# Kernel optimization log

Hardware: AMD Instinct MI355X
Metric: run time of the kernel (lower is better)

Reference implementation:

```python
import jax, jax.numpy as jnp
import numpy as np

ENC = 512            # encoder_image_size
RADIUS = 5.0         # user_input_circle_radius
B, Q, P = 4, 8, 4
IN_H, IN_W = 1024, 1024


def setup_inputs() -> dict:
    key = jax.random.key(0)
    k1, k2, k3 = jax.random.split(key, 3)
    batched_images = jax.random.uniform(k1, (B, 3, IN_H, IN_W), dtype=jnp.float32)
    # points in pixel coordinates of the input image
    batched_points = jax.random.uniform(k2, (B, Q, P, 2), dtype=jnp.float32) * jnp.float32(IN_W)
    batched_point_labels = jax.random.randint(k3, (B, Q, P), 0, 4, dtype=jnp.int32)
    pixel_mean = jnp.array([0.485, 0.456, 0.406], dtype=jnp.float32).reshape(1, 3, 1, 1)
    pixel_std = jnp.array([0.229, 0.224, 0.225], dtype=jnp.float32).reshape(1, 3, 1, 1)
    return {
        "batched_images": batched_images,
        "batched_points": batched_points,
        "batched_point_labels": batched_point_labels,
        "pixel_mean": pixel_mean,
        "pixel_std": pixel_std,
    }


def _early_fusion(batched_images, batched_points, batched_point_labels, pixel_mean, pixel_std):
    b, _, in_h, in_w = batched_images.shape
    q = batched_points.shape[1]
    S = ENC
    # preprocess: bilinear resize (align_corners=False) + normalize
    x = jax.image.resize(batched_images, (b, 3, S, S), method="bilinear", antialias=False)
    x = (x - pixel_mean) / pixel_std
    # rescale points to encoder resolution, keeping negatives at -1
    px = jnp.where(batched_points[..., 0] >= 0, batched_points[..., 0] * (S / in_w), -1.0)
    py = jnp.where(batched_points[..., 1] >= 0, batched_points[..., 1] * (S / in_h), -1.0)
    pts = jnp.stack([px, py], axis=-1)                      # [B,Q,P,2]

    rows = jnp.arange(S, dtype=jnp.float32)                 # row ids (y)
    cols = jnp.arange(S, dtype=jnp.float32)                 # col ids (x)

    # bbox mask from first two points if label[...,0] != 1, else full image
    is_bbox = (batched_point_labels[:, :, 0] != 1).astype(jnp.float32)   # [B,Q]
    tlx = is_bbox * jnp.min(pts[:, :, :2, 0], axis=-1)
    tly = is_bbox * jnp.min(pts[:, :, :2, 1], axis=-1)
    brx = is_bbox * jnp.max(pts[:, :, :2, 0], axis=-1) + (1.0 - is_bbox) * S
    bry = is_bbox * jnp.max(pts[:, :, :2, 1], axis=-1) + (1.0 - is_bbox) * S
    row_within = (rows[None, None, :, None] >= tly[:, :, None, None]) & (rows[None, None, :, None] <= bry[:, :, None, None])
    col_within = (cols[None, None, None, :] >= tlx[:, :, None, None]) & (cols[None, None, None, :] <= brx[:, :, None, None])
    bbox_mask = (row_within & col_within).astype(x.dtype)   # [B,Q,S,S]

    # point (circle) mask: min over points of squared distance, gated by label==1
    is_point = (batched_point_labels == 1).astype(jnp.float32)[:, :, None, None, :]   # [B,Q,1,1,P]
    dx = cols[None, None, None, :, None] - pts[:, :, None, None, :, 0]  # [B,Q,1,S,P]
    dy = rows[None, None, :, None, None] - pts[:, :, None, None, :, 1]  # [B,Q,S,1,P]
    d2 = dx * dx + dy * dy                                               # [B,Q,S,S,P]
    r2 = RADIUS * RADIUS
    gated = d2 * is_point + (1.0 - is_point) * (r2 + 1.0)
    pts_mask = (jnp.min(gated, axis=-1) <= r2).astype(x.dtype)          # [B,Q,S,S]

    imgs = jnp.broadcast_to(x[:, None], (b, q, 3, S, S))
    fused = jnp.concatenate([imgs, bbox_mask[:, :, None], pts_mask[:, :, None]], axis=2)
    return fused.reshape(b * q, 5, S, S)


def reference(batched_images, batched_points, batched_point_labels, pixel_mean, pixel_std):
    return _early_fusion(batched_images, batched_points, batched_point_labels, pixel_mean, pixel_std)
```

## Files before the change

kernel.cpp:

```cpp
#include <hip/hip_runtime.h>

#define S_ENC 512
#define IN_WH 1024
#define NB 4
#define NQ 8
#define NPTS 4
#define PLANE_STRIDE (5 * S_ENC * S_ENC)

typedef float f32x4 __attribute__((ext_vector_type(4)));

__global__ __launch_bounds__(256) void early_fusion_kernel(
    const float* __restrict__ img,
    const float* __restrict__ pts,
    const int*   __restrict__ labels,
    const float* __restrict__ mean,
    const float* __restrict__ stdv,
    float* __restrict__ out)
{
  const int job = blockIdx.y;
  const int tid = blockIdx.x * 256 + threadIdx.x;
  const int y   = tid >> 7;
  const int x4  = (tid & 127) << 2;

  if (job < NB * 3) {
    const int bc = job;
    const int b  = bc / 3;
    const int c  = bc % 3;
    const float m = mean[c];
    const float s = stdv[c];

    const float* in0 =
        img + ((size_t)bc * IN_WH + (size_t)(2 * y)) * IN_WH + 2 * x4;
    const f32x4 a0 = __builtin_nontemporal_load((const f32x4*)(in0));
    const f32x4 a1 = __builtin_nontemporal_load((const f32x4*)(in0 + 4));
    const f32x4 b0 = __builtin_nontemporal_load((const f32x4*)(in0 + IN_WH));
    const f32x4 b1 = __builtin_nontemporal_load((const f32x4*)(in0 + IN_WH + 4));

    f32x4 r;
    r.x = 0.5f * (0.5f * (a0.x + a0.y) + 0.5f * (b0.x + b0.y));
    r.y = 0.5f * (0.5f * (a0.z + a0.w) + 0.5f * (b0.z + b0.w));
    r.z = 0.5f * (0.5f * (a1.x + a1.y) + 0.5f * (b1.x + b1.y));
    r.w = 0.5f * (0.5f * (a1.z + a1.w) + 0.5f * (b1.z + b1.w));
    r.x = (r.x - m) / s;
    r.y = (r.y - m) / s;
    r.z = (r.z - m) / s;
    r.w = (r.w - m) / s;

    float* dst = out + ((size_t)(b * NQ * 5 + c) * S_ENC + y) * S_ENC + x4;
#pragma unroll
    for (int q = 0; q < NQ; ++q) {
      __builtin_nontemporal_store(r, (f32x4*)dst);
      dst += PLANE_STRIDE;
    }
  } else {
    const int idx = job - NB * 3;
    const int bq  = idx >> 1;
    const int c   = 3 + (idx & 1);

    const float* p   = pts + (size_t)bq * NPTS * 2;
    const int*   lab = labels + (size_t)bq * NPTS;
    float px[NPTS], py[NPTS];
    int   lb[NPTS];
#pragma unroll
    for (int i = 0; i < NPTS; ++i) {
      const float vx = p[2 * i + 0];
      const float vy = p[2 * i + 1];
      px[i] = (vx >= 0.0f) ? __fmul_rn(vx, 0.5f) : -1.0f;
      py[i] = (vy >= 0.0f) ? __fmul_rn(vy, 0.5f) : -1.0f;
      lb[i] = lab[i];
    }
    const float fy = (float)y;
    f32x4 r;

    if (c == 3) {
      float tlx, tly, brx, bry;
      if (lb[0] != 1) {
        tlx = fminf(px[0], px[1]);
        tly = fminf(py[0], py[1]);
        brx = fmaxf(px[0], px[1]);
        bry = fmaxf(py[0], py[1]);
      } else {
        tlx = 0.0f; tly = 0.0f;
        brx = (float)S_ENC; bry = (float)S_ENC;
      }
      const bool rowok = (fy >= tly) && (fy <= bry);
#pragma unroll
      for (int j = 0; j < 4; ++j) {
        const float fx = (float)(x4 + j);
        r[j] = (rowok && fx >= tlx && fx <= brx) ? 1.0f : 0.0f;
      }
    } else {
#pragma unroll
      for (int j = 0; j < 4; ++j) {
        const float fx = (float)(x4 + j);
        float mind = 26.0f;
#pragma unroll
        for (int i = 0; i < NPTS; ++i) {
          if (lb[i] == 1) {
            const float dx = __fsub_rn(fx, px[i]);
            const float dy = __fsub_rn(fy, py[i]);
            const float d2 = __fadd_rn(__fmul_rn(dx, dx), __fmul_rn(dy, dy));
            mind = fminf(mind, d2);
          }
        }
        r[j] = (mind <= 25.0f) ? 1.0f : 0.0f;
      }
    }

    __builtin_nontemporal_store(
        r, (f32x4*)(out + ((size_t)(bq * 5 + c) * S_ENC + y) * S_ENC + x4));
  }
}

extern "C" void kernel_launch(void* const* d_in, const int* in_sizes, int n_in,
                              void* d_out, int out_size, void* d_ws, size_t ws_size,
                              hipStream_t stream) {
  const float* img    = (const float*)d_in[0];
  const float* pts    = (const float*)d_in[1];
  const int*   labels = (const int*)d_in[2];
  const float* mean   = (const float*)d_in[3];
  const float* stdv   = (const float*)d_in[4];
  float* out = (float*)d_out;

  dim3 grid(256, NB * 3 + NB * NQ * 2);
  early_fusion_kernel<<<grid, 256, 0, stream>>>(img, pts, labels, mean, stdv, out);
}
```

Baseline: 40.48 us.

## Flatten grid, drop nontemporal hints, widen mask work per thread

Replaces the 2D grid with a 1D grid where image blocks come first and mask jobs use 64 blocks each, with every mask thread writing four float4 chunks 128 columns apart. Nontemporal loads and stores are swapped for ordinary vector loads and stores. The aim is to cut the number of mask blocks and their per-block setup (point and label loads), and to let normal caching handle the write-heavy output. The cost is less parallelism in the mask phase and possible cache pollution from the regular stores.

After: 36.08 us. 1.12x faster.

```diff
diff --git a/kernel.cpp b/kernel.cpp
--- a/kernel.cpp
+++ b/kernel.cpp
@@ -9,6 +9,12 @@
 
 typedef float f32x4 __attribute__((ext_vector_type(4)));
 
+#define IMG_JOBS   (NB * 3)
+#define IMG_BLOCKS (IMG_JOBS * 256)
+#define MASK_JOBS  (NB * NQ * 2)
+#define MASK_BLK_PER_JOB 64
+#define MASK_BLOCKS (MASK_JOBS * MASK_BLK_PER_JOB)
+
 __global__ __launch_bounds__(256) void early_fusion_kernel(
     const float* __restrict__ img,
     const float* __restrict__ pts,
@@ -17,24 +23,24 @@
     const float* __restrict__ stdv,
     float* __restrict__ out)
 {
-  const int job = blockIdx.y;
-  const int tid = blockIdx.x * 256 + threadIdx.x;
-  const int y   = tid >> 7;
-  const int x4  = (tid & 127) << 2;
+  const int bx = blockIdx.x;
 
-  if (job < NB * 3) {
-    const int bc = job;
-    const int b  = bc / 3;
-    const int c  = bc % 3;
+  if (bx < IMG_BLOCKS) {
+    const int bc  = bx >> 8;
+    const int tid = ((bx & 255) << 8) + threadIdx.x;
+    const int y   = tid >> 7;
+    const int x4  = (tid & 127) << 2;
+    const int b   = bc / 3;
+    const int c   = bc % 3;
     const float m = mean[c];
     const float s = stdv[c];
 
     const float* in0 =
         img + ((size_t)bc * IN_WH + (size_t)(2 * y)) * IN_WH + 2 * x4;
-    const f32x4 a0 = __builtin_nontemporal_load((const f32x4*)(in0));
-    const f32x4 a1 = __builtin_nontemporal_load((const f32x4*)(in0 + 4));
-    const f32x4 b0 = __builtin_nontemporal_load((const f32x4*)(in0 + IN_WH));
-    const f32x4 b1 = __builtin_nontemporal_load((const f32x4*)(in0 + IN_WH + 4));
+    const f32x4 a0 = *(const f32x4*)(in0);
+    const f32x4 a1 = *(const f32x4*)(in0 + 4);
+    const f32x4 b0 = *(const f32x4*)(in0 + IN_WH);
+    const f32x4 b1 = *(const f32x4*)(in0 + IN_WH + 4);
 
     f32x4 r;
     r.x = 0.5f * (0.5f * (a0.x + a0.y) + 0.5f * (b0.x + b0.y));
@@ -49,13 +55,17 @@
     float* dst = out + ((size_t)(b * NQ * 5 + c) * S_ENC + y) * S_ENC + x4;
 #pragma unroll
     for (int q = 0; q < NQ; ++q) {
-      __builtin_nontemporal_store(r, (f32x4*)dst);
+      *(f32x4*)dst = r;
       dst += PLANE_STRIDE;
     }
   } else {
-    const int idx = job - NB * 3;
+    const int mb  = bx - IMG_BLOCKS;
+    const int idx = mb >> 6;
     const int bq  = idx >> 1;
     const int c   = 3 + (idx & 1);
+    const int tid = ((mb & 63) << 8) + threadIdx.x;
+    const int y   = tid >> 5;
+    const int x4  = (tid & 31) << 2;
 
     const float* p   = pts + (size_t)bq * NPTS * 2;
     const int*   lab = labels + (size_t)bq * NPTS;
@@ -70,7 +80,7 @@
       lb[i] = lab[i];
     }
     const float fy = (float)y;
-    f32x4 r;
+    float* row = out + ((size_t)(bq * 5 + c) * S_ENC + y) * S_ENC + x4;
 
     if (c == 3) {
       float tlx, tly, brx, bry;
@@ -86,29 +96,36 @@
       const bool rowok = (fy >= tly) && (fy <= bry);
 #pragma unroll
       for (int j = 0; j < 4; ++j) {
-        const float fx = (float)(x4 + j);
-        r[j] = (rowok && fx >= tlx && fx <= brx) ? 1.0f : 0.0f;
+        f32x4 r;
+#pragma unroll
+        for (int e = 0; e < 4; ++e) {
+          const float fx = (float)(x4 + j * 128 + e);
+          r[e] = (rowok && fx >= tlx && fx <= brx) ? 1.0f : 0.0f;
+        }
+        *(f32x4*)(row + j * 128) = r;
       }
     } else {
 #pragma unroll
       for (int j = 0; j < 4; ++j) {
-        const float fx = (float)(x4 + j);
-        float mind = 26.0f;
+        f32x4 r;
 #pragma unroll
-        for (int i = 0; i < NPTS; ++i) {
-          if (lb[i] == 1) {
-            const float dx = __fsub_rn(fx, px[i]);
-            const float dy = __fsub_rn(fy, py[i]);
-            const float d2 = __fadd_rn(__fmul_rn(dx, dx), __fmul_rn(dy, dy));
-            mind = fminf(mind, d2);
+        for (int e = 0; e < 4; ++e) {
+          const float fx = (float)(x4 + j * 128 + e);
+          float mind = 26.0f;
+#pragma unroll
+          for (int i = 0; i < NPTS; ++i) {
+            if (lb[i] == 1) {
+              const float dx = __fsub_rn(fx, px[i]);
+              const float dy = __fsub_rn(fy, py[i]);
+              const float d2 = __fadd_rn(__fmul_rn(dx, dx), __fmul_rn(dy, dy));
+              mind = fminf(mind, d2);
+            }
           }
+          r[e] = (mind <= 25.0f) ? 1.0f : 0.0f;
         }
-        r[j] = (mind <= 25.0f) ? 1.0f : 0.0f;
+        *(f32x4*)(row + j * 128) = r;
       }
     }
-
-    __builtin_nontemporal_store(
-        r, (f32x4*)(out + ((size_t)(bq * 5 + c) * S_ENC + y) * S_ENC + x4));
   }
 }
 
@@ -122,6 +139,6 @@
   const float* stdv   = (const float*)d_in[4];
   float* out = (float*)d_out;
 
-  dim3 grid(256, NB * 3 + NB * NQ * 2);
-  early_fusion_kernel<<<grid, 256, 0, stream>>>(img, pts, labels, mean, stdv, out);
+  early_fusion_kernel<<<dim3(IMG_BLOCKS + MASK_BLOCKS), 256, 0, stream>>>(
+      img, pts, labels, mean, stdv, out);
 }
```
